# Optimization experiments

Hardware: AMD Instinct MI355X
Metric: run time of the kernel (lower is better)

Reference implementation:

```python
import jax, jax.numpy as jnp
import numpy as np

B, S, V, D, H, L = 32, 512, 32000, 512, 256, 9
START, STOP = L, L + 1  # flair-style augmented tagset


def setup_inputs() -> dict:
    key = jax.random.key(0)
    ks = jax.random.split(key, 12)
    input_ids = jax.random.randint(ks[0], (B, S), 0, V)
    input_lens = jax.random.randint(ks[1], (B,), S // 2, S + 1)
    attention_mask = (jnp.arange(S)[None, :] < input_lens[:, None]).astype(jnp.int32)
    labels = jax.random.randint(ks[2], (B, S), 0, L)
    emb_table = jax.random.normal(ks[3], (V, D), jnp.float32) * 0.02
    # stacked LSTM params: [layer, direction, ...]; layer0 in-dim D == layer1 in-dim 2H == 512
    w_ih = jax.random.normal(ks[4], (2, 2, 4 * H, D), jnp.float32) * 0.05
    w_hh = jax.random.normal(ks[5], (2, 2, 4 * H, H), jnp.float32) * 0.05
    b_ih = jax.random.normal(ks[6], (2, 2, 4 * H), jnp.float32) * 0.05
    b_hh = jax.random.normal(ks[7], (2, 2, 4 * H), jnp.float32) * 0.05
    ln_gamma = jnp.ones((2 * H,), jnp.float32)
    ln_beta = jnp.zeros((2 * H,), jnp.float32)
    cls_w = jax.random.normal(ks[8], (L, 2 * H), jnp.float32) * 0.05
    cls_b = jnp.zeros((L,), jnp.float32)
    transitions = jax.random.normal(ks[9], (L + 2, L + 2), jnp.float32) * 0.1
    return dict(input_ids=input_ids, attention_mask=attention_mask,
                input_lens=input_lens, labels=labels, emb_table=emb_table,
                w_ih=w_ih, w_hh=w_hh, b_ih=b_ih, b_hh=b_hh,
                ln_gamma=ln_gamma, ln_beta=ln_beta, cls_w=cls_w, cls_b=cls_b,
                transitions=transitions)


def _lstm_dir(x, wih, whh, bih, bhh, reverse):
    # x: [S, B, in]; PyTorch gate order i, f, g, o
    n = x.shape[1]
    h0 = jnp.zeros((n, whh.shape[1]), x.dtype)

    def step(carry, xt):
        h, c = carry
        g = xt @ wih.T + h @ whh.T + bih + bhh
        i, f, gg, o = jnp.split(g, 4, axis=-1)
        c = jax.nn.sigmoid(f) * c + jax.nn.sigmoid(i) * jnp.tanh(gg)
        h = jax.nn.sigmoid(o) * jnp.tanh(c)
        return (h, c), h

    _, hs = jax.lax.scan(step, (h0, h0), x, reverse=reverse)
    return hs  # [S, B, H], time-aligned with input


def _logits(input_ids, attention_mask, emb_table, w_ih, w_hh, b_ih, b_hh,
            ln_gamma, ln_beta, cls_w, cls_b):
    embs = emb_table[input_ids] * attention_mask[:, :, None].astype(jnp.float32)  # [B,S,D]
    x = jnp.swapaxes(embs, 0, 1)  # [S,B,D]
    for l in range(2):
        fwd = _lstm_dir(x, w_ih[l, 0], w_hh[l, 0], b_ih[l, 0], b_hh[l, 0], False)
        bwd = _lstm_dir(x, w_ih[l, 1], w_hh[l, 1], b_ih[l, 1], b_hh[l, 1], True)
        x = jnp.concatenate([fwd, bwd], axis=-1)  # [S,B,2H]
    seq = jnp.swapaxes(x, 0, 1)  # [B,S,2H]
    mu = seq.mean(-1, keepdims=True)
    var = ((seq - mu) ** 2).mean(-1, keepdims=True)
    seq = (seq - mu) / jnp.sqrt(var + 1e-5) * ln_gamma + ln_beta
    return seq @ cls_w.T + cls_b  # [B,S,L]


def _crf_nll(logits, labels, input_lens, transitions):
    mask = jnp.arange(S)[None, :] < input_lens[:, None]  # [B,S] bool
    trans = transitions[:L, :L]
    # forward algorithm (log partition)
    alpha0 = transitions[START, :L][None, :] + logits[:, 0]  # [B,L]

    def step(alpha, inp):
        e_t, m_t = inp  # [B,L], [B]
        new = jax.nn.logsumexp(alpha[:, :, None] + trans[None, :, :], axis=1) + e_t
        return jnp.where(m_t[:, None], new, alpha), None

    emit_rest = jnp.swapaxes(logits[:, 1:], 0, 1)  # [S-1,B,L]
    mask_rest = mask[:, 1:].T
    alpha, _ = jax.lax.scan(step, alpha0, (emit_rest, mask_rest))
    logZ = jax.nn.logsumexp(alpha + transitions[:L, STOP][None, :], axis=1)  # [B]
    # gold path score
    mf = mask.astype(logits.dtype)
    emit_score = jnp.sum(
        jnp.take_along_axis(logits, labels[:, :, None], axis=2)[:, :, 0] * mf, axis=1)
    trans_score = jnp.sum(trans[labels[:, :-1], labels[:, 1:]] * mf[:, 1:], axis=1)
    y_last = jnp.take_along_axis(labels, (input_lens - 1)[:, None], axis=1)[:, 0]
    gold = (emit_score + trans_score
            + transitions[START, labels[:, 0]] + transitions[y_last, STOP])
    return jnp.mean(logZ - gold)


def reference(input_ids, attention_mask, input_lens, labels, emb_table,
              w_ih, w_hh, b_ih, b_hh, ln_gamma, ln_beta, cls_w, cls_b,
              transitions):
    logits = _logits(input_ids, attention_mask, emb_table, w_ih, w_hh, b_ih,
                     b_hh, ln_gamma, ln_beta, cls_w, cls_b)
    loss = _crf_nll(logits, labels, input_lens, transitions)
    return (loss, logits)
```

## Files before the change

kernel.cpp:

```cpp
#include <hip/hip_runtime.h>

#define B_ 32
#define S_ 512
#define D_ 512
#define H_ 256

typedef float floatx4 __attribute__((ext_vector_type(4)));
typedef short short8v __attribute__((ext_vector_type(8)));
typedef int intx4 __attribute__((ext_vector_type(4)));
typedef unsigned short u16;
typedef unsigned int u32;
typedef unsigned long long u64;

#define WS_NEEDED 138575872ull

__device__ __forceinline__ u16 f2bf(float f) {
  u32 x = __float_as_uint(f);
  x += 0x7fffu + ((x >> 16) & 1u);
  return (u16)(x >> 16);
}
__device__ __forceinline__ float bf2f(u16 h) {
  return __uint_as_float(((u32)h) << 16);
}
__device__ __forceinline__ float decode_hl(u32 v) {
  return bf2f((u16)(v >> 16)) + bf2f((u16)(v & 0xffffu));
}
__device__ __forceinline__ float sigf(float x) {
  return 1.0f / (1.0f + __expf(-x));
}
__device__ __forceinline__ float tanh_f(float x) {
  float e = __expf(-2.0f * fabsf(x));
  float r = (1.0f - e) / (1.0f + e);
  return copysignf(r, x);
}
__device__ __forceinline__ float rcp_f(float x) {
  float r; asm("v_rcp_f32 %0, %1" : "=v"(r) : "v"(x)); return r;
}
__device__ __forceinline__ float sig_fast(float x) {
  return rcp_f(1.0f + __expf(-x));
}
__device__ __forceinline__ float tanh_fast(float x) {
  float e = __expf(-2.0f * fabsf(x));
  float r = (1.0f - e) * rcp_f(1.0f + e);
  return copysignf(r, x);
}

struct alignas(16) U16x8 { u16 v[8]; };

__global__ void prep_k(const int* __restrict__ ids, const int* __restrict__ amask,
                       const float* __restrict__ emb, u16* __restrict__ X0) {
  int m = blockIdx.x;
  int lane = threadIdx.x;
  int s = m >> 5, b = m & 31;
  int id = ids[b * S_ + s];
  int mk = amask[b * S_ + s];
  const float4* src = (const float4*)(emb + (size_t)id * D_) + lane * 2;
  float4 v0 = src[0], v1 = src[1];
  if (!mk) { v0 = make_float4(0,0,0,0); v1 = make_float4(0,0,0,0); }
  U16x8 o;
  o.v[0]=f2bf(v0.x); o.v[1]=f2bf(v0.y); o.v[2]=f2bf(v0.z); o.v[3]=f2bf(v0.w);
  o.v[4]=f2bf(v1.x); o.v[5]=f2bf(v1.y); o.v[6]=f2bf(v1.z); o.v[7]=f2bf(v1.w);
  *(U16x8*)(X0 + (size_t)m * D_ + lane * 8) = o;
}

__global__ void conv_k(const float* __restrict__ w, u16* __restrict__ wbf, int n8) {
  int idx = blockIdx.x * blockDim.x + threadIdx.x;
  if (idx >= n8) return;
  const float4* s = (const float4*)w + (size_t)idx * 2;
  float4 v0 = s[0], v1 = s[1];
  U16x8 o;
  o.v[0]=f2bf(v0.x); o.v[1]=f2bf(v0.y); o.v[2]=f2bf(v0.z); o.v[3]=f2bf(v0.w);
  o.v[4]=f2bf(v1.x); o.v[5]=f2bf(v1.y); o.v[6]=f2bf(v1.z); o.v[7]=f2bf(v1.w);
  *(U16x8*)(wbf + (size_t)idx * 8) = o;
}

__global__ void zero_k(float* __restrict__ loss) {
  if (threadIdx.x == 0) *loss = 0.f;
}

__global__ void convw_k(const float* __restrict__ whh, signed char* __restrict__ wq,
                        float* __restrict__ wsc) {
  const int r = blockIdx.x;
  const int lane = threadIdx.x;
  float4 v = *(const float4*)(whh + (size_t)r * 256 + lane * 4);
  float m = fmaxf(fmaxf(fabsf(v.x), fabsf(v.y)), fmaxf(fabsf(v.z), fabsf(v.w)));
  #pragma unroll
  for (int off = 32; off > 0; off >>= 1) m = fmaxf(m, __shfl_xor(m, off, 64));
  const float s = fmaxf(m, 1e-20f) * (1.0f / 127.0f);
  const float inv = 1.0f / s;
  int q0 = (int)rintf(v.x * inv), q1 = (int)rintf(v.y * inv);
  int q2 = (int)rintf(v.z * inv), q3 = (int)rintf(v.w * inv);
  u32 pk = (u32)(q0 & 255) | ((u32)(q1 & 255) << 8)
         | ((u32)(q2 & 255) << 16) | ((u32)(q3 & 255) << 24);
  *(u32*)(wq + (size_t)r * 256 + lane * 4) = pk;
  if (lane == 0) wsc[r] = s * (1.0f / 127.0f);
}

__global__ void gemm_k(const u16* __restrict__ A, const u16* __restrict__ W,
                       const float* __restrict__ bih, const float* __restrict__ bhh,
                       u16* __restrict__ G) {
  __shared__ short Asm[64 * 40];
  __shared__ short Bsm[64 * 40];
  const int tid = threadIdx.x;
  const int m0 = blockIdx.x * 64, n0 = blockIdx.y * 64;
  const int wid = tid >> 6, lane = tid & 63;
  const int quad = lane >> 4, lr = lane & 15;
  const int wm = (wid >> 1) * 32, wn = (wid & 1) * 32;
  const int lrow = tid >> 2, lk = (tid & 3) * 8;
  floatx4 acc00 = {0,0,0,0}, acc01 = {0,0,0,0}, acc10 = {0,0,0,0}, acc11 = {0,0,0,0};
  for (int kt = 0; kt < 16; ++kt) {
    const int k0 = kt * 32;
    uint4 av = *(const uint4*)(A + (size_t)(m0 + lrow) * 512 + k0 + lk);
    uint4 bv = *(const uint4*)(W + (size_t)(n0 + lrow) * 512 + k0 + lk);
    __syncthreads();
    *(uint4*)&Asm[lrow * 40 + lk] = av;
    *(uint4*)&Bsm[lrow * 40 + lk] = bv;
    __syncthreads();
    short8v a0 = *(const short8v*)&Asm[(wm + lr) * 40 + quad * 8];
    short8v a1 = *(const short8v*)&Asm[(wm + 16 + lr) * 40 + quad * 8];
    short8v b0 = *(const short8v*)&Bsm[(wn + lr) * 40 + quad * 8];
    short8v b1 = *(const short8v*)&Bsm[(wn + 16 + lr) * 40 + quad * 8];
    acc00 = __builtin_amdgcn_mfma_f32_16x16x32_bf16(a0, b0, acc00, 0, 0, 0);
    acc01 = __builtin_amdgcn_mfma_f32_16x16x32_bf16(a0, b1, acc01, 0, 0, 0);
    acc10 = __builtin_amdgcn_mfma_f32_16x16x32_bf16(a1, b0, acc10, 0, 0, 0);
    acc11 = __builtin_amdgcn_mfma_f32_16x16x32_bf16(a1, b1, acc11, 0, 0, 0);
  }
  #pragma unroll
  for (int j = 0; j < 2; ++j) {
    const int n = n0 + wn + j * 16 + lr;
    const float bias = bih[n] + bhh[n];
    #pragma unroll
    for (int i = 0; i < 2; ++i) {
      const int mb = m0 + wm + i * 16 + quad * 4;
      floatx4 av = (i == 0) ? (j == 0 ? acc00 : acc01) : (j == 0 ? acc10 : acc11);
      #pragma unroll
      for (int rr = 0; rr < 4; ++rr) {
        G[(size_t)(mb + rr) * 2048 + n] = f2bf(av[rr] + bias);
      }
    }
  }
}

__launch_bounds__(512, 2)
__global__ void rec_k(const u16* __restrict__ G, const signed char* __restrict__ wq_l,
                      const float* __restrict__ wsc_l,
                      u16* __restrict__ Xbf, u32* __restrict__ Xu) {
  __shared__ alignas(16) signed char hq[2][4][256];

  const int tid = threadIdx.x;
  const int dir = blockIdx.x >> 3;
  const int bg = blockIdx.x & 7;
  const int w = tid >> 6;
  const int lane = tid & 63;
  const int q = lane >> 4;
  const int c = lane & 15;
  const int b4 = c & 3;
  const int s = (c >> 2) & 1;
  const int r0 = ((c >> 3) & 1) * 2;

  const signed char* wq = wq_l + (size_t)dir * 262144;
  const float* wsc = wsc_l + (size_t)dir * 1024;

  intx4 A[4][2][4];
  #pragma unroll
  for (int g = 0; g < 4; ++g)
    #pragma unroll
    for (int s_ = 0; s_ < 2; ++s_) {
      const int row = g * 256 + w * 32 + s_ * 16 + c;
      #pragma unroll
      for (int kt = 0; kt < 4; ++kt)
        A[g][s_][kt] = *(const intx4*)(wq + (size_t)row * 256 + kt * 64 + q * 16);
    }
  float sc[4][2];
  #pragma unroll
  for (int g = 0; g < 4; ++g)
    #pragma unroll
    for (int k = 0; k < 2; ++k)
      sc[g][k] = wsc[g * 256 + w * 32 + s * 16 + q * 4 + r0 + k];

  if (tid < 128) ((uint4*)hq)[tid] = make_uint4(0, 0, 0, 0);
  float cst[2] = {0.f, 0.f};

  const u16* gb_ = G + (size_t)(bg * 4 + b4) * 2048 + dir * 1024
                 + w * 32 + s * 16 + q * 4 + r0;
  u32 gc[4], gn[4];
  #pragma unroll
  for (int pf = 0; pf < 2; ++pf) {
    const int tn = dir ? (511 - pf) : pf;
    const u16* gp = gb_ + (size_t)tn * 65536;
    u32* dst = pf ? gn : gc;
    dst[0] = *(const u32*)(gp);
    dst[1] = *(const u32*)(gp + 256);
    dst[2] = *(const u32*)(gp + 512);
    dst[3] = *(const u32*)(gp + 768);
  }
  __syncthreads();

  for (int st = 0; st < 512; ++st) {
    const int par = st & 1;
    const signed char* hrow = &hq[par][b4][0];
    intx4 bf0 = *(const intx4*)&hrow[((0 * 4 + q) ^ b4) * 16];
    intx4 bf1 = *(const intx4*)&hrow[((1 * 4 + q) ^ b4) * 16];
    intx4 bf2 = *(const intx4*)&hrow[((2 * 4 + q) ^ b4) * 16];
    intx4 bf3 = *(const intx4*)&hrow[((3 * 4 + q) ^ b4) * 16];
    intx4 acc[4][2];
    #pragma unroll
    for (int g = 0; g < 4; ++g)
      #pragma unroll
      for (int s_ = 0; s_ < 2; ++s_) {
        intx4 a_ = {0, 0, 0, 0};
        a_ = __builtin_amdgcn_mfma_i32_16x16x64_i8(A[g][s_][0], bf0, a_, 0, 0, 0);
        a_ = __builtin_amdgcn_mfma_i32_16x16x64_i8(A[g][s_][1], bf1, a_, 0, 0, 0);
        a_ = __builtin_amdgcn_mfma_i32_16x16x64_i8(A[g][s_][2], bf2, a_, 0, 0, 0);
        a_ = __builtin_amdgcn_mfma_i32_16x16x64_i8(A[g][s_][3], bf3, a_, 0, 0, 0);
        acc[g][s_] = a_;
      }
    intx4 x0 = s ? acc[0][1] : acc[0][0];
    intx4 x1 = s ? acc[1][1] : acc[1][0];
    intx4 x2 = s ? acc[2][1] : acc[2][0];
    intx4 x3 = s ? acc[3][1] : acc[3][0];
    u16 hb16[2]; float hfv[2];
    #pragma unroll
    for (int k = 0; k < 2; ++k) {
      const float a0v = (float)(r0 ? x0[2 + k] : x0[k]);
      const float a1v = (float)(r0 ? x1[2 + k] : x1[k]);
      const float a2v = (float)(r0 ? x2[2 + k] : x2[k]);
      const float a3v = (float)(r0 ? x3[2 + k] : x3[k]);
      const float si = bf2f((u16)(gc[0] >> (16 * k))) + a0v * sc[0][k];
      const float sf = bf2f((u16)(gc[1] >> (16 * k))) + a1v * sc[1][k];
      const float sg = bf2f((u16)(gc[2] >> (16 * k))) + a2v * sc[2][k];
      const float so = bf2f((u16)(gc[3] >> (16 * k))) + a3v * sc[3][k];
      const float ig = sig_fast(si), fg = sig_fast(sf);
      const float gg = tanh_fast(sg), og = sig_fast(so);
      const float cn = fg * cst[k] + ig * gg;
      const float hn = og * tanh_fast(cn);
      cst[k] = cn;
      hfv[k] = hn;
      hb16[k] = f2bf(hn);
    }
    {
      const int q0v = (int)rintf(hfv[0] * 127.f);
      const int q1v = (int)rintf(hfv[1] * 127.f);
      const u16 pk = (u16)((q0v & 255) | ((q1v & 255) << 8));
      const int chunk = 2 * w + s;
      *(u16*)((signed char*)hq + (size_t)(par ^ 1) * 1024 + b4 * 256
              + ((chunk ^ b4) * 16) + q * 4 + r0) = pk;
    }
    {
      const int tt = dir ? (511 - st) : st;
      const size_t xo = ((size_t)tt * 32 + bg * 4 + b4) * 512 + dir * 256
                      + w * 32 + s * 16 + q * 4 + r0;
      if (Xbf) {
        *(u32*)(Xbf + xo) = (u32)hb16[0] | ((u32)hb16[1] << 16);
      } else {
        u32 xa = ((u32)hb16[0] << 16) | f2bf(hfv[0] - bf2f(hb16[0]));
        u32 xb = ((u32)hb16[1] << 16) | f2bf(hfv[1] - bf2f(hb16[1]));
        *(u64*)(Xu + xo) = (u64)xa | ((u64)xb << 32);
      }
    }
    gc[0] = gn[0]; gc[1] = gn[1]; gc[2] = gn[2]; gc[3] = gn[3];
    {
      const int stn = (st + 2 < 512) ? st + 2 : 511;
      const int tn = dir ? (511 - stn) : stn;
      const u16* gp = gb_ + (size_t)tn * 65536;
      gn[0] = *(const u32*)(gp);
      gn[1] = *(const u32*)(gp + 256);
      gn[2] = *(const u32*)(gp + 512);
      gn[3] = *(const u32*)(gp + 768);
    }
    asm volatile("s_waitcnt lgkmcnt(0)" ::: "memory");
    __builtin_amdgcn_s_barrier();
    __builtin_amdgcn_sched_barrier(0);
  }
}

__global__ void head_k(const u32* __restrict__ X2u, const float* __restrict__ gamma,
                       const float* __restrict__ beta, const float* __restrict__ cw,
                       const float* __restrict__ cb, float* __restrict__ out) {
  __shared__ float red[9][64];
  const int m = blockIdx.x, lane = threadIdx.x;
  const int s = m >> 5, b = m & 31;
  const uint4* xp = (const uint4*)(X2u + (size_t)m * 512) + lane * 2;
  uint4 a0 = xp[0], a1 = xp[1];
  float x[8];
  x[0] = decode_hl(a0.x); x[1] = decode_hl(a0.y);
  x[2] = decode_hl(a0.z); x[3] = decode_hl(a0.w);
  x[4] = decode_hl(a1.x); x[5] = decode_hl(a1.y);
  x[6] = decode_hl(a1.z); x[7] = decode_hl(a1.w);
  float sm = 0.f, sq = 0.f;
  #pragma unroll
  for (int i = 0; i < 8; ++i) { sm += x[i]; sq += x[i] * x[i]; }
  #pragma unroll
  for (int off = 32; off > 0; off >>= 1) {
    sm += __shfl_xor(sm, off, 64);
    sq += __shfl_xor(sq, off, 64);
  }
  const float mu = sm * (1.0f / 512.0f);
  const float var = sq * (1.0f / 512.0f) - mu * mu;
  const float rs = rsqrtf(var + 1e-5f);
  const float4* gp = (const float4*)gamma + lane * 2;
  const float4* bp = (const float4*)beta + lane * 2;
  float4 g0 = gp[0], g1 = gp[1], be0 = bp[0], be1 = bp[1];
  float nv[8];
  nv[0] = (x[0] - mu) * rs * g0.x + be0.x;
  nv[1] = (x[1] - mu) * rs * g0.y + be0.y;
  nv[2] = (x[2] - mu) * rs * g0.z + be0.z;
  nv[3] = (x[3] - mu) * rs * g0.w + be0.w;
  nv[4] = (x[4] - mu) * rs * g1.x + be1.x;
  nv[5] = (x[5] - mu) * rs * g1.y + be1.y;
  nv[6] = (x[6] - mu) * rs * g1.z + be1.z;
  nv[7] = (x[7] - mu) * rs * g1.w + be1.w;
  #pragma unroll
  for (int c = 0; c < 9; ++c) {
    const float4* wp = (const float4*)(cw + (size_t)c * 512) + lane * 2;
    float4 w0 = wp[0], w1 = wp[1];
    red[c][lane] = nv[0]*w0.x + nv[1]*w0.y + nv[2]*w0.z + nv[3]*w0.w
                 + nv[4]*w1.x + nv[5]*w1.y + nv[6]*w1.z + nv[7]*w1.w;
  }
  __syncthreads();
  if (lane < 9) {
    float t = 0.f;
    for (int i = 0; i < 64; ++i) t += red[lane][i];
    out[1 + ((size_t)b * 512 + s) * 9 + lane] = t + cb[lane];
  }
}

__global__ void crf_k(const float* __restrict__ logits, const int* __restrict__ labels,
                      const int* __restrict__ lens, const float* __restrict__ tr,
                      float* __restrict__ loss) {
  const int b = blockIdx.x, lane = threadIdx.x;
  const int len = lens[b];
  float trj[9];
  #pragma unroll
  for (int i = 0; i < 9; ++i) trj[i] = 0.f;
  if (lane < 9) {
    #pragma unroll
    for (int i = 0; i < 9; ++i) trj[i] = tr[i * 11 + lane];
  }
  float alpha = -1e30f;
  if (lane < 9) alpha = tr[9 * 11 + lane] + logits[(size_t)b * 512 * 9 + lane];
  for (int t = 1; t < len; ++t) {
    float e = (lane < 9) ? logits[((size_t)b * 512 + t) * 9 + lane] : 0.f;
    float v[9];
    float mx = -1e30f;
    #pragma unroll
    for (int i = 0; i < 9; ++i) {
      v[i] = __shfl(alpha, i, 64) + trj[i];
      mx = fmaxf(mx, v[i]);
    }
    float ss = 0.f;
    #pragma unroll
    for (int i = 0; i < 9; ++i) ss += __expf(v[i] - mx);
    float na = mx + __logf(ss) + e;
    if (lane < 9) alpha = na;
  }
  float fin = (lane < 9) ? alpha + tr[lane * 11 + 10] : -1e30f;
  float mx = fin;
  #pragma unroll
  for (int off = 8; off > 0; off >>= 1) mx = fmaxf(mx, __shfl_xor(mx, off, 64));
  float es = (lane < 9) ? __expf(fin - mx) : 0.f;
  #pragma unroll
  for (int off = 8; off > 0; off >>= 1) es += __shfl_xor(es, off, 64);
  const float logZ = mx + __logf(es);
  float emit = 0.f, ts = 0.f;
  for (int t = lane; t < len; t += 64) {
    int y = labels[b * 512 + t];
    emit += logits[((size_t)b * 512 + t) * 9 + y];
  }
  for (int t = 1 + lane; t < len; t += 64) {
    int y0 = labels[b * 512 + t - 1], y1 = labels[b * 512 + t];
    ts += tr[y0 * 11 + y1];
  }
  #pragma unroll
  for (int off = 32; off > 0; off >>= 1) {
    emit += __shfl_xor(emit, off, 64);
    ts += __shfl_xor(ts, off, 64);
  }
  if (lane == 0) {
    int y0 = labels[b * 512], yl = labels[b * 512 + len - 1];
    float gold = emit + ts + tr[9 * 11 + y0] + tr[yl * 11 + 10];
    atomicAdd(loss, (logZ - gold) * (1.0f / 32.0f));
  }
}

extern "C" void kernel_launch(void* const* d_in, const int* in_sizes, int n_in,
                              void* d_out, int out_size, void* d_ws, size_t ws_size,
                              hipStream_t stream) {
  const int* ids = (const int*)d_in[0];
  const int* amask = (const int*)d_in[1];
  const int* lens = (const int*)d_in[2];
  const int* labels = (const int*)d_in[3];
  const float* emb = (const float*)d_in[4];
  const float* w_ih = (const float*)d_in[5];
  const float* w_hh = (const float*)d_in[6];
  const float* b_ih = (const float*)d_in[7];
  const float* b_hh = (const float*)d_in[8];
  const float* gamma = (const float*)d_in[9];
  const float* beta = (const float*)d_in[10];
  const float* cw = (const float*)d_in[11];
  const float* cb = (const float*)d_in[12];
  const float* tr = (const float*)d_in[13];
  (void)in_sizes; (void)n_in; (void)out_size;

  if (ws_size < WS_NEEDED) return;

  char* p = (char*)d_ws;
  u16* X0 = (u16*)p;      p += (size_t)16384 * 512 * 2;
  u16* Wbf = (u16*)p;     p += (size_t)2 * 2 * 1024 * 512 * 2;
  u16* G = (u16*)p;       p += (size_t)16384 * 2048 * 2;
  u16* X1 = (u16*)p;      p += (size_t)16384 * 512 * 2;
  u32* X2u = (u32*)p;     p += (size_t)16384 * 512 * 4;
  float* out = (float*)d_out;

  signed char* Wq = (signed char*)X0;
  float* Wsc = (float*)((char*)X0 + 1048576);

  prep_k<<<16384, 64, 0, stream>>>(ids, amask, emb, X0);
  conv_k<<<1024, 256, 0, stream>>>(w_ih, Wbf, 262144);
  zero_k<<<1, 64, 0, stream>>>(out);
  gemm_k<<<dim3(256, 32), 256, 0, stream>>>(X0, Wbf, b_ih, b_hh, G);
  convw_k<<<4096, 64, 0, stream>>>(w_hh, Wq, Wsc);
  rec_k<<<16, 512, 0, stream>>>(G, Wq, Wsc, X1, nullptr);
  gemm_k<<<dim3(256, 32), 256, 0, stream>>>(X1, Wbf + 2 * 1024 * 512,
                                            b_ih + 2048, b_hh + 2048, G);
  rec_k<<<16, 512, 0, stream>>>(G, Wq + 2 * 262144, Wsc + 2048, nullptr, X2u);
  head_k<<<16384, 64, 0, stream>>>(X2u, gamma, beta, cw, cb, out);
  crf_k<<<32, 64, 0, stream>>>(out + 1, labels, lens, tr, out);
}
```

Baseline: 1.503 ms.

## Split LSTM recurrence across twice as many blocks with two batches each

The recurrent kernel now handles two batch rows per block instead of four, launching 32 blocks instead of 16 per layer. Each lane computes one hidden unit for one batch row rather than two, which shortens the serial per-step elementwise gate work. The MFMA count per step is unchanged, but half of each MFMA's batch columns are now duplicated, and global loads and stores shrink to 16-bit granularity. It relies on idle CUs to absorb the extra blocks and makes wider use of the 16-column MFMA tile.

```diff
diff --git a/kernel.cpp b/kernel.cpp
--- a/kernel.cpp
+++ b/kernel.cpp
@@ -43,6 +43,11 @@
   float e = __expf(-2.0f * fabsf(x));
   float r = (1.0f - e) * rcp_f(1.0f + e);
   return copysignf(r, x);
+}
+__device__ __forceinline__ int sel4(intx4 v, int r) {
+  const int lo = (r & 1) ? v[1] : v[0];
+  const int hi = (r & 1) ? v[3] : v[2];
+  return (r & 2) ? hi : lo;
 }
 
 struct alignas(16) U16x8 { u16 v[8]; };
@@ -145,18 +150,18 @@
 __global__ void rec_k(const u16* __restrict__ G, const signed char* __restrict__ wq_l,
                       const float* __restrict__ wsc_l,
                       u16* __restrict__ Xbf, u32* __restrict__ Xu) {
-  __shared__ alignas(16) signed char hq[2][4][256];
+  __shared__ alignas(16) signed char hq[2][2][256];
 
   const int tid = threadIdx.x;
-  const int dir = blockIdx.x >> 3;
-  const int bg = blockIdx.x & 7;
+  const int dir = blockIdx.x >> 4;
+  const int bg = blockIdx.x & 15;
   const int w = tid >> 6;
   const int lane = tid & 63;
   const int q = lane >> 4;
   const int c = lane & 15;
-  const int b4 = c & 3;
-  const int s = (c >> 2) & 1;
-  const int r0 = ((c >> 3) & 1) * 2;
+  const int b2 = c & 1;
+  const int s = (c >> 1) & 1;
+  const int r = c >> 2;
 
   const signed char* wq = wq_l + (size_t)dir * 262144;
   const float* wsc = wsc_l + (size_t)dir * 1024;
@@ -171,38 +176,35 @@
       for (int kt = 0; kt < 4; ++kt)
         A[g][s_][kt] = *(const intx4*)(wq + (size_t)row * 256 + kt * 64 + q * 16);
     }
-  float sc[4][2];
-  #pragma unroll
-  for (int g = 0; g < 4; ++g)
-    #pragma unroll
-    for (int k = 0; k < 2; ++k)
-      sc[g][k] = wsc[g * 256 + w * 32 + s * 16 + q * 4 + r0 + k];
-
-  if (tid < 128) ((uint4*)hq)[tid] = make_uint4(0, 0, 0, 0);
-  float cst[2] = {0.f, 0.f};
-
-  const u16* gb_ = G + (size_t)(bg * 4 + b4) * 2048 + dir * 1024
-                 + w * 32 + s * 16 + q * 4 + r0;
-  u32 gc[4], gn[4];
+  const int hid = w * 32 + s * 16 + q * 4 + r;
+  float sc[4];
+  #pragma unroll
+  for (int g = 0; g < 4; ++g) sc[g] = wsc[g * 256 + hid];
+
+  if (tid < 64) ((uint4*)hq)[tid] = make_uint4(0, 0, 0, 0);
+  float cst = 0.f;
+
+  const u16* gb_ = G + (size_t)(bg * 2 + b2) * 2048 + dir * 1024 + hid;
+  u16 gc[4], gn[4];
   #pragma unroll
   for (int pf = 0; pf < 2; ++pf) {
     const int tn = dir ? (511 - pf) : pf;
     const u16* gp = gb_ + (size_t)tn * 65536;
-    u32* dst = pf ? gn : gc;
-    dst[0] = *(const u32*)(gp);
-    dst[1] = *(const u32*)(gp + 256);
-    dst[2] = *(const u32*)(gp + 512);
-    dst[3] = *(const u32*)(gp + 768);
+    u16* dst = pf ? gn : gc;
+    dst[0] = gp[0];
+    dst[1] = gp[256];
+    dst[2] = gp[512];
+    dst[3] = gp[768];
   }
   __syncthreads();
 
   for (int st = 0; st < 512; ++st) {
     const int par = st & 1;
-    const signed char* hrow = &hq[par][b4][0];
-    intx4 bf0 = *(const intx4*)&hrow[((0 * 4 + q) ^ b4) * 16];
-    intx4 bf1 = *(const intx4*)&hrow[((1 * 4 + q) ^ b4) * 16];
-    intx4 bf2 = *(const intx4*)&hrow[((2 * 4 + q) ^ b4) * 16];
-    intx4 bf3 = *(const intx4*)&hrow[((3 * 4 + q) ^ b4) * 16];
+    const signed char* hrow = &hq[par][b2][0];
+    intx4 bf0 = *(const intx4*)&hrow[((0 * 4 + q) ^ b2) * 16];
+    intx4 bf1 = *(const intx4*)&hrow[((1 * 4 + q) ^ b2) * 16];
+    intx4 bf2 = *(const intx4*)&hrow[((2 * 4 + q) ^ b2) * 16];
+    intx4 bf3 = *(const intx4*)&hrow[((3 * 4 + q) ^ b2) * 16];
     intx4 acc[4][2];
     #pragma unroll
     for (int g = 0; g < 4; ++g)
@@ -215,47 +217,33 @@
         a_ = __builtin_amdgcn_mfma_i32_16x16x64_i8(A[g][s_][3], bf3, a_, 0, 0, 0);
         acc[g][s_] = a_;
       }
-    intx4 x0 = s ? acc[0][1] : acc[0][0];
-    intx4 x1 = s ? acc[1][1] : acc[1][0];
-    intx4 x2 = s ? acc[2][1] : acc[2][0];
-    intx4 x3 = s ? acc[3][1] : acc[3][0];
-    u16 hb16[2]; float hfv[2];
-    #pragma unroll
-    for (int k = 0; k < 2; ++k) {
-      const float a0v = (float)(r0 ? x0[2 + k] : x0[k]);
-      const float a1v = (float)(r0 ? x1[2 + k] : x1[k]);
-      const float a2v = (float)(r0 ? x2[2 + k] : x2[k]);
-      const float a3v = (float)(r0 ? x3[2 + k] : x3[k]);
-      const float si = bf2f((u16)(gc[0] >> (16 * k))) + a0v * sc[0][k];
-      const float sf = bf2f((u16)(gc[1] >> (16 * k))) + a1v * sc[1][k];
-      const float sg = bf2f((u16)(gc[2] >> (16 * k))) + a2v * sc[2][k];
-      const float so = bf2f((u16)(gc[3] >> (16 * k))) + a3v * sc[3][k];
-      const float ig = sig_fast(si), fg = sig_fast(sf);
-      const float gg = tanh_fast(sg), og = sig_fast(so);
-      const float cn = fg * cst[k] + ig * gg;
-      const float hn = og * tanh_fast(cn);
-      cst[k] = cn;
-      hfv[k] = hn;
-      hb16[k] = f2bf(hn);
-    }
+    const int v0 = sel4(s ? acc[0][1] : acc[0][0], r);
+    const int v1 = sel4(s ? acc[1][1] : acc[1][0], r);
+    const int v2 = sel4(s ? acc[2][1] : acc[2][0], r);
+    const int v3 = sel4(s ? acc[3][1] : acc[3][0], r);
+    const float si = bf2f(gc[0]) + (float)v0 * sc[0];
+    const float sf = bf2f(gc[1]) + (float)v1 * sc[1];
+    const float sg = bf2f(gc[2]) + (float)v2 * sc[2];
+    const float so = bf2f(gc[3]) + (float)v3 * sc[3];
+    const float ig = sig_fast(si), fg = sig_fast(sf);
+    const float gg = tanh_fast(sg), og = sig_fast(so);
+    const float cn = fg * cst + ig * gg;
+    const float hn = og * tanh_fast(cn);
+    cst = cn;
+    const u16 hb = f2bf(hn);
     {
-      const int q0v = (int)rintf(hfv[0] * 127.f);
-      const int q1v = (int)rintf(hfv[1] * 127.f);
-      const u16 pk = (u16)((q0v & 255) | ((q1v & 255) << 8));
+      const int qv = (int)rintf(hn * 127.f);
       const int chunk = 2 * w + s;
-      *(u16*)((signed char*)hq + (size_t)(par ^ 1) * 1024 + b4 * 256
-              + ((chunk ^ b4) * 16) + q * 4 + r0) = pk;
+      ((signed char*)hq)[(size_t)(par ^ 1) * 512 + b2 * 256
+                         + ((chunk ^ b2) * 16) + q * 4 + r] = (signed char)qv;
     }
     {
       const int tt = dir ? (511 - st) : st;
-      const size_t xo = ((size_t)tt * 32 + bg * 4 + b4) * 512 + dir * 256
-                      + w * 32 + s * 16 + q * 4 + r0;
+      const size_t xo = ((size_t)tt * 32 + bg * 2 + b2) * 512 + dir * 256 + hid;
       if (Xbf) {
-        *(u32*)(Xbf + xo) = (u32)hb16[0] | ((u32)hb16[1] << 16);
+        *(u16*)(Xbf + xo) = hb;
       } else {
-        u32 xa = ((u32)hb16[0] << 16) | f2bf(hfv[0] - bf2f(hb16[0]));
-        u32 xb = ((u32)hb16[1] << 16) | f2bf(hfv[1] - bf2f(hb16[1]));
-        *(u64*)(Xu + xo) = (u64)xa | ((u64)xb << 32);
+        *(u32*)(Xu + xo) = ((u32)hb << 16) | f2bf(hn - bf2f(hb));
       }
     }
     gc[0] = gn[0]; gc[1] = gn[1]; gc[2] = gn[2]; gc[3] = gn[3];
@@ -263,10 +251,10 @@
       const int stn = (st + 2 < 512) ? st + 2 : 511;
       const int tn = dir ? (511 - stn) : stn;
       const u16* gp = gb_ + (size_t)tn * 65536;
-      gn[0] = *(const u32*)(gp);
-      gn[1] = *(const u32*)(gp + 256);
-      gn[2] = *(const u32*)(gp + 512);
-      gn[3] = *(const u32*)(gp + 768);
+      gn[0] = gp[0];
+      gn[1] = gp[256];
+      gn[2] = gp[512];
+      gn[3] = gp[768];
     }
     asm volatile("s_waitcnt lgkmcnt(0)" ::: "memory");
     __builtin_amdgcn_s_barrier();
@@ -420,10 +408,10 @@
   zero_k<<<1, 64, 0, stream>>>(out);
   gemm_k<<<dim3(256, 32), 256, 0, stream>>>(X0, Wbf, b_ih, b_hh, G);
   convw_k<<<4096, 64, 0, stream>>>(w_hh, Wq, Wsc);
-  rec_k<<<16, 512, 0, stream>>>(G, Wq, Wsc, X1, nullptr);
+  rec_k<<<32, 512, 0, stream>>>(G, Wq, Wsc, X1, nullptr);
   gemm_k<<<dim3(256, 32), 256, 0, stream>>>(X1, Wbf + 2 * 1024 * 512,
                                             b_ih + 2048, b_hh + 2048, G);
-  rec_k<<<16, 512, 0, stream>>>(G, Wq + 2 * 262144, Wsc + 2048, nullptr, X2u);
+  rec_k<<<32, 512, 0, stream>>>(G, Wq + 2 * 262144, Wsc + 2048, nullptr, X2u);
   head_k<<<16384, 64, 0, stream>>>(X2u, gamma, beta, cw, cb, out);
   crf_k<<<32, 64, 0, stream>>>(out + 1, labels, lens, tr, out);
 }
```

New measurement: 1.288 ms. 14.3% less time.
